# Performance work log

Measured on AMD Instinct MI355X. Metric: run time of the kernel, lower is better.

The kernel has to match this reference:

```python
import jax, jax.numpy as jnp
import numpy as np

B, P, D, K, OUT = 16, 2048, 64, 16, 128


def setup_inputs() -> dict:
    key = jax.random.key(0)
    k1, k2, k3 = jax.random.split(key, 3)
    x = jax.random.normal(k1, (B * P, D), dtype=jnp.float32)
    pos = jax.random.normal(k2, (B * P, 3), dtype=jnp.float32)
    batch = jnp.repeat(jnp.arange(B, dtype=jnp.int64), P)  # sorted segment ids
    # Linear(2*D -> OUT), torch convention W: [out, in]
    W = jax.random.normal(k3, (OUT, 2 * D), dtype=jnp.float32) / np.sqrt(2 * D)
    b = jnp.zeros((OUT,), dtype=jnp.float32)
    return {"x": x, "pos": pos, "batch": batch, "W": W, "b": b}


def _knn_idx(xb):
    # xb: [P, D] one cloud; returns [P, K] indices of K nearest neighbors (self excluded)
    sq = jnp.sum(xb * xb, axis=-1)  # [P]
    d2 = sq[:, None] + sq[None, :] - 2.0 * (xb @ xb.T)  # [P, P]
    d2 = d2 + jnp.eye(P, dtype=xb.dtype) * jnp.asarray(1e10, xb.dtype)  # loop=False
    _, idx = jax.lax.top_k(-d2, K)  # smallest distances
    return idx


def reference(x, pos, batch, W, b):
    # batch is uniform segments of size P (sorted), so reshape is equivalent
    xb = x.reshape(B, P, D)
    idx = jax.vmap(_knn_idx)(xb)  # [B, P, K]
    # gather neighbor features per cloud
    xj = jax.vmap(lambda f, i: f[i])(xb, idx)  # [B, P, K, D]
    xi = jnp.broadcast_to(xb[:, :, None, :], (B, P, K, D))
    e = jnp.concatenate([xi, xj - xi], axis=-1)  # [B, P, K, 2D]
    h = jnp.einsum('bpkd,od->bpko', e, W) + b  # edge MLP
    out = jnp.max(h, axis=2)  # max aggregation over neighbors -> [B, P, OUT]
    out = jax.nn.relu(out)
    return out.reshape(B * P, OUT)
```

## Files before the change

kernel.cpp:

```cpp
#include <hip/hip_runtime.h>

typedef __bf16 bf16x8 __attribute__((ext_vector_type(8)));
typedef float  f32x4  __attribute__((ext_vector_type(4)));

#define NBAT 16
#define NP   2048
#define ND   64
#define NOUT 128
#define NK   16
#define RT   16
#define HSTR 2052

static __device__ __forceinline__ unsigned short f2bf(float f) {
    unsigned u = __float_as_uint(f);
    u += 0x7FFF + ((u >> 16) & 1);
    return (unsigned short)(u >> 16);
}
static __device__ __forceinline__ int lanes_below(unsigned long long m) {
    return (int)__builtin_amdgcn_mbcnt_hi((unsigned)(m >> 32),
             __builtin_amdgcn_mbcnt_lo((unsigned)m, 0u));
}
static __device__ __forceinline__ unsigned long long umin64(unsigned long long a, unsigned long long b){ return a < b ? a : b; }
static __device__ __forceinline__ unsigned long long umax64(unsigned long long a, unsigned long long b){ return a < b ? b : a; }

static __device__ __forceinline__ void bitonic_sort128_u64(unsigned long long &k0,
                                                           unsigned long long &k1, int lane) {
#pragma unroll
    for (int k = 2; k <= 64; k <<= 1) {
#pragma unroll
        for (int j = k >> 1; j >= 1; j >>= 1) {
            bool lower = ((lane & j) == 0);
            bool up0 = (k == 64) ? true  : ((lane & k) == 0);
            bool up1 = (k == 64) ? false : ((lane & k) == 0);
            unsigned long long o0 = __shfl_xor(k0, j, 64);
            k0 = (up0 == lower) ? umin64(k0, o0) : umax64(k0, o0);
            unsigned long long o1 = __shfl_xor(k1, j, 64);
            k1 = (up1 == lower) ? umin64(k1, o1) : umax64(k1, o1);
        }
    }
    { unsigned long long mn = umin64(k0, k1), mx = umax64(k0, k1); k0 = mn; k1 = mx; }
#pragma unroll
    for (int j = 32; j >= 1; j >>= 1) {
        bool lower = ((lane & j) == 0);
        unsigned long long o0 = __shfl_xor(k0, j, 64);
        k0 = lower ? umin64(k0, o0) : umax64(k0, o0);
        unsigned long long o1 = __shfl_xor(k1, j, 64);
        k1 = lower ? umin64(k1, o1) : umax64(k1, o1);
    }
}

static __device__ __forceinline__ float
refine_d(const float* __restrict__ x, int gr, int gcbase, int jc) {
    const float* xr = x + (size_t)gr * ND;
    const float* xc = x + (size_t)(gcbase + jc) * ND;
    double s0 = 0.0, s1 = 0.0;
#pragma unroll
    for (int k8 = 0; k8 < 8; ++k8) {
        float4 a = *(const float4*)(xr + k8 * 8);
        float4 b = *(const float4*)(xc + k8 * 8);
        float4 a2 = *(const float4*)(xr + k8 * 8 + 4);
        float4 b2 = *(const float4*)(xc + k8 * 8 + 4);
        double e0 = (double)a.x - (double)b.x;
        double e1 = (double)a.y - (double)b.y;
        double e2 = (double)a.z - (double)b.z;
        double e3 = (double)a.w - (double)b.w;
        s0 = fma(e0, e0, s0); s0 = fma(e1, e1, s0);
        s0 = fma(e2, e2, s0); s0 = fma(e3, e3, s0);
        double f0 = (double)a2.x - (double)b2.x;
        double f1 = (double)a2.y - (double)b2.y;
        double f2 = (double)a2.z - (double)b2.z;
        double f3 = (double)a2.w - (double)b2.w;
        s1 = fma(f0, f0, s1); s1 = fma(f1, f1, s1);
        s1 = fma(f2, f2, s1); s1 = fma(f3, f3, s1);
    }
    return (float)(s0 + s1);
}

static __device__ __forceinline__ void cvt_hilo(const float* __restrict__ p,
                                                bf16x8 &hi, bf16x8 &lo) {
    float4 a = *(const float4*)p, b = *(const float4*)(p + 4);
    float f[8] = {a.x, a.y, a.z, a.w, b.x, b.y, b.z, b.w};
#pragma unroll
    for (int i = 0; i < 8; ++i) {
        __bf16 h = (__bf16)f[i];
        hi[i] = h;
        lo[i] = (__bf16)(f[i] - (float)h);
    }
}

__global__ void __launch_bounds__(256)
prep_k(const float* __restrict__ x,
       const float* __restrict__ W,
       const float* __restrict__ bias,
       float* __restrict__ sq, float* __restrict__ U,
       float* __restrict__ V,  unsigned short* __restrict__ xb16)
{
    const int blk = blockIdx.x, tid = threadIdx.x;
    const int R0b = blk * 64;
    const int w  = tid >> 6, l = tid & 63;
    const int l15 = l & 15, lg = l >> 4, kc = lg * 8;

    bf16x8 wh[2][4], wl[2][4];
#pragma unroll
    for (int tt = 0; tt < 2; ++tt) {
        const float* wb = W + (size_t)((w + tt * 4) * 16 + l15) * (2 * ND) + kc;
#pragma unroll
        for (int p = 0; p < 4; ++p)
            cvt_hilo(wb + p * 32, wh[tt][p], wl[tt][p]);
    }
    const int o0a = w * 16 + lg * 4;
    const int o0b = (w + 4) * 16 + lg * 4;
    float4 boa = *(const float4*)(bias + o0a);
    float4 bob = *(const float4*)(bias + o0b);

#pragma unroll 1
    for (int s4 = 0; s4 < 4; ++s4) {
        const int R0 = R0b + s4 * 16;

        {
            int r = tid >> 4, c = (tid & 15) * 4;
            float4 v = *(const float4*)(x + (size_t)(R0 + r) * ND + c);
            ushort4 hb;
            hb.x = f2bf(v.x); hb.y = f2bf(v.y); hb.z = f2bf(v.z); hb.w = f2bf(v.w);
            *(ushort4*)(xb16 + (size_t)(R0 + r) * ND + c) = hb;
        }
        if (tid < 128) {
            int r = tid >> 3, seg = tid & 7;
            const float* p = x + (size_t)(R0 + r) * ND + seg * 8;
            float4 a = *(const float4*)(p);
            float4 b = *(const float4*)(p + 4);
            double s = (double)a.x * a.x + (double)a.y * a.y +
                       (double)a.z * a.z + (double)a.w * a.w +
                       (double)b.x * b.x + (double)b.y * b.y +
                       (double)b.z * b.z + (double)b.w * b.w;
            s += __shfl_xor(s, 1, 64);
            s += __shfl_xor(s, 2, 64);
            s += __shfl_xor(s, 4, 64);
            if (seg == 0) sq[R0 + r] = (float)s;
        }

        const float* xr = x + (size_t)(R0 + l15) * ND + kc;
        bf16x8 bh0, bl0, bh1, bl1;
        cvt_hilo(xr,      bh0, bl0);
        cvt_hilo(xr + 32, bh1, bl1);

#pragma unroll
        for (int tt = 0; tt < 2; ++tt) {
            f32x4 accP = {0.f, 0.f, 0.f, 0.f};
            f32x4 accV = {0.f, 0.f, 0.f, 0.f};
            accP = __builtin_amdgcn_mfma_f32_16x16x32_bf16(wh[tt][0], bh0, accP, 0, 0, 0);
            accP = __builtin_amdgcn_mfma_f32_16x16x32_bf16(wh[tt][0], bl0, accP, 0, 0, 0);
            accP = __builtin_amdgcn_mfma_f32_16x16x32_bf16(wl[tt][0], bh0, accP, 0, 0, 0);
            accP = __builtin_amdgcn_mfma_f32_16x16x32_bf16(wh[tt][1], bh1, accP, 0, 0, 0);
            accP = __builtin_amdgcn_mfma_f32_16x16x32_bf16(wh[tt][1], bl1, accP, 0, 0, 0);
            accP = __builtin_amdgcn_mfma_f32_16x16x32_bf16(wl[tt][1], bh1, accP, 0, 0, 0);
            accV = __builtin_amdgcn_mfma_f32_16x16x32_bf16(wh[tt][2], bh0, accV, 0, 0, 0);
            accV = __builtin_amdgcn_mfma_f32_16x16x32_bf16(wh[tt][2], bl0, accV, 0, 0, 0);
            accV = __builtin_amdgcn_mfma_f32_16x16x32_bf16(wl[tt][2], bh0, accV, 0, 0, 0);
            accV = __builtin_amdgcn_mfma_f32_16x16x32_bf16(wh[tt][3], bh1, accV, 0, 0, 0);
            accV = __builtin_amdgcn_mfma_f32_16x16x32_bf16(wh[tt][3], bl1, accV, 0, 0, 0);
            accV = __builtin_amdgcn_mfma_f32_16x16x32_bf16(wl[tt][3], bh1, accV, 0, 0, 0);

            const int o0 = tt ? o0b : o0a;
            float4 bo = tt ? bob : boa;
            float4 uu, vv;
            uu.x = accP[0] - accV[0] + bo.x;  vv.x = accV[0];
            uu.y = accP[1] - accV[1] + bo.y;  vv.y = accV[1];
            uu.z = accP[2] - accV[2] + bo.z;  vv.z = accV[2];
            uu.w = accP[3] - accV[3] + bo.w;  vv.w = accV[3];
            *(float4*)(U + (size_t)(R0 + l15) * NOUT + o0) = uu;
            *(float4*)(V + (size_t)(R0 + l15) * NOUT + o0) = vv;
        }
    }
}

__global__ void __launch_bounds__(1024, 2)
knn_k(const float* __restrict__ x,
      const unsigned short* __restrict__ xb16,
      const float* __restrict__ sq,
      const float* __restrict__ U,
      const float* __restrict__ V,
      float* __restrict__ out)
{
    extern __shared__ __align__(16) unsigned char smem[];
    unsigned short* d2h = (unsigned short*)smem;
    __shared__ unsigned short cbuf[16][128];

    const int q   = blockIdx.x;
    const int xcd = q & 7;
    const int k_  = q >> 3;
    const int bb  = xcd * 2 + (k_ >> 7);
    const int rt  = k_ & 127;
    const int R0l = rt * RT;
    const int R0g = bb * NP + R0l;
    const int tid = threadIdx.x;
    const int w   = tid >> 6;
    const int l   = tid & 63;
    const int l15 = l & 15, lg = l >> 4, kc = lg * 8;

    const unsigned short* nr = xb16 + (size_t)(R0g + l15) * ND + kc;
    bf16x8 n0 = *(const bf16x8*)(nr);
    bf16x8 n1 = *(const bf16x8*)(nr + 32);
    const float sqrow = sq[R0g + l15];

    const unsigned short* xbb = xb16 + (size_t)bb * NP * ND;
    const float* sqb = sq + bb * NP;

#pragma unroll 4
    for (int t = 0; t < 8; ++t) {
        const int cb = (w * 8 + t) * 16;
        const unsigned short* ar = xbb + (size_t)(cb + l15) * ND + kc;
        bf16x8 a0 = *(const bf16x8*)(ar);
        bf16x8 a1 = *(const bf16x8*)(ar + 32);
        f32x4 acc = {0.f, 0.f, 0.f, 0.f};
        acc = __builtin_amdgcn_mfma_f32_16x16x32_bf16(a0, n0, acc, 0, 0, 0);
        acc = __builtin_amdgcn_mfma_f32_16x16x32_bf16(a1, n1, acc, 0, 0, 0);
        const int jb4 = cb + lg * 4;
        float4 sq4 = *(const float4*)(sqb + jb4);
        unsigned short hh[4];
#pragma unroll
        for (int i = 0; i < 4; ++i) {
            float sqc = (i == 0) ? sq4.x : (i == 1) ? sq4.y : (i == 2) ? sq4.z : sq4.w;
            float d2 = fmaxf(fmaf(-2.f, acc[i], sqrow + sqc), 0.f);
            unsigned short h = __builtin_bit_cast(unsigned short, (_Float16)d2);
            if (R0l + l15 == jb4 + i) h = 0x7C00;
            hh[i] = h;
        }
        ushort4 hv; hv.x = hh[0]; hv.y = hh[1]; hv.z = hh[2]; hv.w = hh[3];
        *(ushort4*)(d2h + (size_t)l15 * HSTR + jb4) = hv;
    }
    __syncthreads();

    const int gcbase = bb * NP;
    {
        const int r  = w;
        const int gr = R0g + r;
        const unsigned short* rowp = d2h + (size_t)r * HSTR;

        unsigned int h[32];
#pragma unroll
        for (int s = 0; s < 8; ++s) {
            ushort4 hv = *(const ushort4*)(rowp + (s * 64 + l) * 4);
            h[s*4+0] = hv.x; h[s*4+1] = hv.y; h[s*4+2] = hv.z; h[s*4+3] = hv.w;
        }
        unsigned int mnh = h[0];
#pragma unroll
        for (int i = 1; i < 32; ++i) mnh = (h[i] < mnh) ? h[i] : mnh;

        unsigned int t16 = 0;
#pragma unroll
        for (int b = 15; b >= 0; --b) {
            unsigned int cand = t16 | (1u << b);
            int c = __popcll(__ballot(mnh < cand));
            if (c < 16) t16 = cand;
        }
        float tf = (float)__builtin_bit_cast(_Float16, (unsigned short)t16) + 1.0f;
        unsigned int tauh =
            (unsigned int)__builtin_bit_cast(unsigned short, (_Float16)tf) + 1u;

        unsigned int packed = 0; int cnt = 0;
#pragma unroll
        for (int i = 0; i < 32; ++i) {
            if (h[i] <= tauh) {
                if (cnt < 4) packed |= (unsigned)i << (5 * cnt);
                ++cnt;
            }
        }
        bool ovf = (__ballot(cnt > 4) != 0ull);

        cbuf[w][l]      = 0xFFFF;
        cbuf[w][64 + l] = 0xFFFF;
        int total;
        if (!ovf) {
            int inc = cnt;
#pragma unroll
            for (int off = 1; off < 64; off <<= 1) {
                int nv = __shfl_up(inc, off, 64);
                if (l >= off) inc += nv;
            }
            int excl = inc - cnt;
            total = __shfl(inc, 63, 64);
#pragma unroll
            for (int kk = 0; kk < 4; ++kk) {
                if (kk < cnt && excl + kk < 128) {
                    int slot = (packed >> (5 * kk)) & 31;
                    cbuf[w][excl + kk] =
                        (unsigned short)(256 * (slot >> 2) + 4 * l + (slot & 3));
                }
            }
        } else {
            int base = 0;
#pragma unroll 1
            for (int i = 0; i < 32; ++i) {
                bool pred = (h[i] <= tauh);
                unsigned long long m = __ballot(pred);
                int pos = base + lanes_below(m);
                if (pred && pos < 128)
                    cbuf[w][pos] = (unsigned short)(256 * (i >> 2) + 4 * l + (i & 3));
                base += __popcll(m);
            }
            total = base;
        }
        asm volatile("s_waitcnt lgkmcnt(0)" ::: "memory");
        __builtin_amdgcn_sched_barrier(0);

        const float* Vb = V + (size_t)bb * NP * NOUT;
        float mv0 = -1e30f, mv1 = -1e30f;
        int jc = cbuf[w][l];

        bool fast = (total <= 64);
        unsigned long long win_m = 0ull;
        if (fast) {
            unsigned int dbits = 0xFFFFFFFFu;
            if (jc != 0xFFFF)
                dbits = __float_as_uint(refine_d(x, gr, gcbase, jc));

            unsigned int T = 0;
#pragma unroll
            for (int b = 30; b >= 0; --b) {
                unsigned int cand = T | (1u << b);
                int c = __popcll(__ballot(dbits < cand));
                if (c < 16) T = cand;
            }
            unsigned long long less_m = __ballot(dbits < T);
            int c_less = __popcll(less_m);
            int need = 16 - c_less;
            unsigned long long tie_m = __ballot(dbits == T);
            if (__popcll(tie_m) == need) {
                win_m = less_m | tie_m;
            } else {
                fast = false;
            }
        }

        if (fast) {
            int jns[NK];
            unsigned long long mm = win_m;
#pragma unroll
            for (int n = 0; n < NK; ++n) {
                int ln = __ffsll((long long)mm) - 1;
                jns[n] = __builtin_amdgcn_readlane(jc, ln);
                mm &= mm - 1;
            }
            float2 vv[NK];
#pragma unroll
            for (int n = 0; n < NK; ++n)
                vv[n] = *(const float2*)(Vb + (size_t)jns[n] * NOUT + (l << 1));
#pragma unroll
            for (int n = 0; n < NK; ++n) {
                mv0 = fmaxf(mv0, vv[n].x);
                mv1 = fmaxf(mv1, vv[n].y);
            }
        } else {
            int jc1 = cbuf[w][64 + l];
            unsigned long long rk0 = (jc != 0xFFFF)
                ? ((((unsigned long long)__float_as_uint(refine_d(x, gr, gcbase, jc))) << 11) | (unsigned)jc)
                : ~0ull;
            unsigned long long rk1 = (jc1 != 0xFFFF)
                ? ((((unsigned long long)__float_as_uint(refine_d(x, gr, gcbase, jc1))) << 11) | (unsigned)jc1)
                : ~0ull;
            bitonic_sort128_u64(rk0, rk1, l);
            int nbr = (int)(rk0 & 2047u);
            int jns[NK];
#pragma unroll
            for (int n = 0; n < NK; ++n)
                jns[n] = __builtin_amdgcn_readlane(nbr, n);
            float2 vv[NK];
#pragma unroll
            for (int n = 0; n < NK; ++n)
                vv[n] = *(const float2*)(Vb + (size_t)jns[n] * NOUT + (l << 1));
#pragma unroll
            for (int n = 0; n < NK; ++n) {
                mv0 = fmaxf(mv0, vv[n].x);
                mv1 = fmaxf(mv1, vv[n].y);
            }
        }

        float2 uu = *(const float2*)(U + (size_t)gr * NOUT + (l << 1));
        float2 ov;
        ov.x = fmaxf(uu.x + mv0, 0.f);
        ov.y = fmaxf(uu.y + mv1, 0.f);
        *(float2*)(out + (size_t)gr * NOUT + (l << 1)) = ov;
    }
}

extern "C" void kernel_launch(void* const* d_in, const int* in_sizes, int n_in,
                              void* d_out, int out_size, void* d_ws, size_t ws_size,
                              hipStream_t stream) {
    const float* x    = (const float*)d_in[0];
    const float* W    = (const float*)d_in[3];
    const float* bias = (const float*)d_in[4];
    float* out = (float*)d_out;

    float* sq = (float*)d_ws;
    float* U  = sq + NBAT * NP;
    float* V  = U  + (size_t)NBAT * NP * NOUT;
    unsigned short* xb16 = (unsigned short*)(V + (size_t)NBAT * NP * NOUT);

    prep_k<<<512, 256, 0, stream>>>(x, W, bias, sq, U, V, xb16);

    const int lds_bytes = RT * HSTR * 2;
    (void)hipFuncSetAttribute((const void*)knn_k,
                        hipFuncAttributeMaxDynamicSharedMemorySize, lds_bytes);
    knn_k<<<2048, 1024, lds_bytes, stream>>>(x, xb16, sq, U, V, out);
}
```

Before: 159.5 us.

## Halve knn block to 8 waves, each handling two rows with interleaved selection

The knn kernel now launches 512 threads per block instead of 1024. Each wave computes 16 column tiles of the distance matrix instead of 8, and later selects neighbours for two query rows at once, interleaving the ballot searches, the fp64 refinement and the V gathers for both rows to expose more ILP. The coarse threshold search now runs over 10 bits of the fp16 key instead of 16. This cuts per-row serial ballot latency and fits more blocks per CU, but raises register pressure, and the fallback path now runs serially over both rows whenever either row misses the fast path.

```diff
diff --git a/kernel.cpp b/kernel.cpp
--- a/kernel.cpp
+++ b/kernel.cpp
@@ -56,8 +56,8 @@
     double s0 = 0.0, s1 = 0.0;
 #pragma unroll
     for (int k8 = 0; k8 < 8; ++k8) {
-        float4 a = *(const float4*)(xr + k8 * 8);
-        float4 b = *(const float4*)(xc + k8 * 8);
+        float4 a  = *(const float4*)(xr + k8 * 8);
+        float4 b  = *(const float4*)(xc + k8 * 8);
         float4 a2 = *(const float4*)(xr + k8 * 8 + 4);
         float4 b2 = *(const float4*)(xc + k8 * 8 + 4);
         double e0 = (double)a.x - (double)b.x;
@@ -116,7 +116,6 @@
 #pragma unroll 1
     for (int s4 = 0; s4 < 4; ++s4) {
         const int R0 = R0b + s4 * 16;
-
         {
             int r = tid >> 4, c = (tid & 15) * 4;
             float4 v = *(const float4*)(x + (size_t)(R0 + r) * ND + c);
@@ -138,12 +137,10 @@
             s += __shfl_xor(s, 4, 64);
             if (seg == 0) sq[R0 + r] = (float)s;
         }
-
         const float* xr = x + (size_t)(R0 + l15) * ND + kc;
         bf16x8 bh0, bl0, bh1, bl1;
         cvt_hilo(xr,      bh0, bl0);
         cvt_hilo(xr + 32, bh1, bl1);
-
 #pragma unroll
         for (int tt = 0; tt < 2; ++tt) {
             f32x4 accP = {0.f, 0.f, 0.f, 0.f};
@@ -160,7 +157,6 @@
             accV = __builtin_amdgcn_mfma_f32_16x16x32_bf16(wh[tt][3], bh1, accV, 0, 0, 0);
             accV = __builtin_amdgcn_mfma_f32_16x16x32_bf16(wh[tt][3], bl1, accV, 0, 0, 0);
             accV = __builtin_amdgcn_mfma_f32_16x16x32_bf16(wl[tt][3], bh1, accV, 0, 0, 0);
-
             const int o0 = tt ? o0b : o0a;
             float4 bo = tt ? bob : boa;
             float4 uu, vv;
@@ -174,7 +170,7 @@
     }
 }
 
-__global__ void __launch_bounds__(1024, 2)
+__global__ void __launch_bounds__(512, 2)
 knn_k(const float* __restrict__ x,
       const unsigned short* __restrict__ xb16,
       const float* __restrict__ sq,
@@ -184,7 +180,7 @@
 {
     extern __shared__ __align__(16) unsigned char smem[];
     unsigned short* d2h = (unsigned short*)smem;
-    __shared__ unsigned short cbuf[16][128];
+    __shared__ unsigned short cbuf[8][2][128];
 
     const int q   = blockIdx.x;
     const int xcd = q & 7;
@@ -207,8 +203,8 @@
     const float* sqb = sq + bb * NP;
 
 #pragma unroll 4
-    for (int t = 0; t < 8; ++t) {
-        const int cb = (w * 8 + t) * 16;
+    for (int t = 0; t < 16; ++t) {
+        const int cb = (w * 16 + t) * 16;
         const unsigned short* ar = xbb + (size_t)(cb + l15) * ND + kc;
         bf16x8 a0 = *(const bf16x8*)(ar);
         bf16x8 a1 = *(const bf16x8*)(ar + 32);
@@ -232,156 +228,265 @@
     __syncthreads();
 
     const int gcbase = bb * NP;
+    const int rA = w, rB = w + 8;
+    const int grA = R0g + rA, grB = R0g + rB;
+    const unsigned short* rpA = d2h + (size_t)rA * HSTR;
+    const unsigned short* rpB = d2h + (size_t)rB * HSTR;
+
+    unsigned int hA[32], hB[32];
+#pragma unroll
+    for (int s = 0; s < 8; ++s) {
+        ushort4 a = *(const ushort4*)(rpA + (s * 64 + l) * 4);
+        ushort4 b = *(const ushort4*)(rpB + (s * 64 + l) * 4);
+        hA[s*4+0] = a.x; hA[s*4+1] = a.y; hA[s*4+2] = a.z; hA[s*4+3] = a.w;
+        hB[s*4+0] = b.x; hB[s*4+1] = b.y; hB[s*4+2] = b.z; hB[s*4+3] = b.w;
+    }
+    unsigned int mnA = hA[0], mnB = hB[0];
+#pragma unroll
+    for (int i = 1; i < 32; ++i) {
+        mnA = (hA[i] < mnA) ? hA[i] : mnA;
+        mnB = (hB[i] < mnB) ? hB[i] : mnB;
+    }
+
+    unsigned int m6A = mnA >> 6, m6B = mnB >> 6;
+    unsigned int tA = 0, tB = 0;
+#pragma unroll
+    for (int b = 9; b >= 0; --b) {
+        unsigned int cA = tA | (1u << b);
+        unsigned int cB = tB | (1u << b);
+        int nA = __popcll(__ballot(m6A < cA));
+        int nB = __popcll(__ballot(m6B < cB));
+        if (nA < 16) tA = cA;
+        if (nB < 16) tB = cB;
+    }
+    float tfA = (float)__builtin_bit_cast(_Float16, (unsigned short)((tA << 6) | 0x3F)) + 1.0f;
+    float tfB = (float)__builtin_bit_cast(_Float16, (unsigned short)((tB << 6) | 0x3F)) + 1.0f;
+    unsigned int tauA = (unsigned int)__builtin_bit_cast(unsigned short, (_Float16)tfA) + 1u;
+    unsigned int tauB = (unsigned int)__builtin_bit_cast(unsigned short, (_Float16)tfB) + 1u;
+
+    unsigned int pkA = 0, pkB = 0; int cntA = 0, cntB = 0;
+#pragma unroll
+    for (int i = 0; i < 32; ++i) {
+        if (hA[i] <= tauA) { if (cntA < 4) pkA |= (unsigned)i << (5 * cntA); ++cntA; }
+        if (hB[i] <= tauB) { if (cntB < 4) pkB |= (unsigned)i << (5 * cntB); ++cntB; }
+    }
+    bool ovfA = (__ballot(cntA > 4) != 0ull);
+    bool ovfB = (__ballot(cntB > 4) != 0ull);
+
+    cbuf[w][0][l] = 0xFFFF; cbuf[w][0][64 + l] = 0xFFFF;
+    cbuf[w][1][l] = 0xFFFF; cbuf[w][1][64 + l] = 0xFFFF;
+    int totA, totB;
     {
-        const int r  = w;
-        const int gr = R0g + r;
-        const unsigned short* rowp = d2h + (size_t)r * HSTR;
-
-        unsigned int h[32];
-#pragma unroll
-        for (int s = 0; s < 8; ++s) {
-            ushort4 hv = *(const ushort4*)(rowp + (s * 64 + l) * 4);
-            h[s*4+0] = hv.x; h[s*4+1] = hv.y; h[s*4+2] = hv.z; h[s*4+3] = hv.w;
-        }
-        unsigned int mnh = h[0];
-#pragma unroll
-        for (int i = 1; i < 32; ++i) mnh = (h[i] < mnh) ? h[i] : mnh;
-
-        unsigned int t16 = 0;
-#pragma unroll
-        for (int b = 15; b >= 0; --b) {
-            unsigned int cand = t16 | (1u << b);
-            int c = __popcll(__ballot(mnh < cand));
-            if (c < 16) t16 = cand;
-        }
-        float tf = (float)__builtin_bit_cast(_Float16, (unsigned short)t16) + 1.0f;
-        unsigned int tauh =
-            (unsigned int)__builtin_bit_cast(unsigned short, (_Float16)tf) + 1u;
-
-        unsigned int packed = 0; int cnt = 0;
-#pragma unroll
-        for (int i = 0; i < 32; ++i) {
-            if (h[i] <= tauh) {
-                if (cnt < 4) packed |= (unsigned)i << (5 * cnt);
-                ++cnt;
-            }
-        }
-        bool ovf = (__ballot(cnt > 4) != 0ull);
-
-        cbuf[w][l]      = 0xFFFF;
-        cbuf[w][64 + l] = 0xFFFF;
-        int total;
-        if (!ovf) {
-            int inc = cnt;
-#pragma unroll
-            for (int off = 1; off < 64; off <<= 1) {
-                int nv = __shfl_up(inc, off, 64);
-                if (l >= off) inc += nv;
-            }
-            int excl = inc - cnt;
-            total = __shfl(inc, 63, 64);
-#pragma unroll
-            for (int kk = 0; kk < 4; ++kk) {
-                if (kk < cnt && excl + kk < 128) {
-                    int slot = (packed >> (5 * kk)) & 31;
-                    cbuf[w][excl + kk] =
-                        (unsigned short)(256 * (slot >> 2) + 4 * l + (slot & 3));
+        int iA = cntA, iB = cntB;
+#pragma unroll
+        for (int off = 1; off < 64; off <<= 1) {
+            int uA = __shfl_up(iA, off, 64);
+            int uB = __shfl_up(iB, off, 64);
+            if (l >= off) { iA += uA; iB += uB; }
+        }
+        int exA = iA - cntA, exB = iB - cntB;
+        totA = __shfl(iA, 63, 64);
+        totB = __shfl(iB, 63, 64);
+        if (!ovfA) {
+#pragma unroll
+            for (int kk = 0; kk < 4; ++kk)
+                if (kk < cntA && exA + kk < 128) {
+                    int s = (pkA >> (5 * kk)) & 31;
+                    cbuf[w][0][exA + kk] = (unsigned short)(256 * (s >> 2) + 4 * l + (s & 3));
                 }
-            }
         } else {
             int base = 0;
 #pragma unroll 1
             for (int i = 0; i < 32; ++i) {
-                bool pred = (h[i] <= tauh);
-                unsigned long long m = __ballot(pred);
+                bool p = (hA[i] <= tauA);
+                unsigned long long m = __ballot(p);
                 int pos = base + lanes_below(m);
-                if (pred && pos < 128)
-                    cbuf[w][pos] = (unsigned short)(256 * (i >> 2) + 4 * l + (i & 3));
+                if (p && pos < 128)
+                    cbuf[w][0][pos] = (unsigned short)(256 * (i >> 2) + 4 * l + (i & 3));
                 base += __popcll(m);
             }
-            total = base;
-        }
-        asm volatile("s_waitcnt lgkmcnt(0)" ::: "memory");
-        __builtin_amdgcn_sched_barrier(0);
-
-        const float* Vb = V + (size_t)bb * NP * NOUT;
-        float mv0 = -1e30f, mv1 = -1e30f;
-        int jc = cbuf[w][l];
-
-        bool fast = (total <= 64);
-        unsigned long long win_m = 0ull;
-        if (fast) {
-            unsigned int dbits = 0xFFFFFFFFu;
-            if (jc != 0xFFFF)
-                dbits = __float_as_uint(refine_d(x, gr, gcbase, jc));
-
-            unsigned int T = 0;
-#pragma unroll
-            for (int b = 30; b >= 0; --b) {
-                unsigned int cand = T | (1u << b);
-                int c = __popcll(__ballot(dbits < cand));
-                if (c < 16) T = cand;
+            totA = base;
+        }
+        if (!ovfB) {
+#pragma unroll
+            for (int kk = 0; kk < 4; ++kk)
+                if (kk < cntB && exB + kk < 128) {
+                    int s = (pkB >> (5 * kk)) & 31;
+                    cbuf[w][1][exB + kk] = (unsigned short)(256 * (s >> 2) + 4 * l + (s & 3));
+                }
+        } else {
+            int base = 0;
+#pragma unroll 1
+            for (int i = 0; i < 32; ++i) {
+                bool p = (hB[i] <= tauB);
+                unsigned long long m = __ballot(p);
+                int pos = base + lanes_below(m);
+                if (p && pos < 128)
+                    cbuf[w][1][pos] = (unsigned short)(256 * (i >> 2) + 4 * l + (i & 3));
+                base += __popcll(m);
             }
-            unsigned long long less_m = __ballot(dbits < T);
-            int c_less = __popcll(less_m);
-            int need = 16 - c_less;
-            unsigned long long tie_m = __ballot(dbits == T);
-            if (__popcll(tie_m) == need) {
-                win_m = less_m | tie_m;
+            totB = base;
+        }
+    }
+    asm volatile("s_waitcnt lgkmcnt(0)" ::: "memory");
+    __builtin_amdgcn_sched_barrier(0);
+
+    const float* Vb = V + (size_t)bb * NP * NOUT;
+    int jcA = cbuf[w][0][l];
+    int jcB = cbuf[w][1][l];
+
+    int jsA = (jcA == 0xFFFF) ? 0 : jcA;
+    int jsB = (jcB == 0xFFFF) ? 0 : jcB;
+    unsigned int dbA, dbB;
+    {
+        const float* xrA = x + (size_t)grA * ND;
+        const float* xcA = x + (size_t)(gcbase + jsA) * ND;
+        const float* xrB = x + (size_t)grB * ND;
+        const float* xcB = x + (size_t)(gcbase + jsB) * ND;
+        double a0 = 0.0, a1 = 0.0, b0 = 0.0, b1 = 0.0;
+#pragma unroll
+        for (int k8 = 0; k8 < 8; ++k8) {
+            float4 ra  = *(const float4*)(xrA + k8 * 8);
+            float4 ca  = *(const float4*)(xcA + k8 * 8);
+            float4 ra2 = *(const float4*)(xrA + k8 * 8 + 4);
+            float4 ca2 = *(const float4*)(xcA + k8 * 8 + 4);
+            float4 rb  = *(const float4*)(xrB + k8 * 8);
+            float4 cb2 = *(const float4*)(xcB + k8 * 8);
+            float4 rb2 = *(const float4*)(xrB + k8 * 8 + 4);
+            float4 cb3 = *(const float4*)(xcB + k8 * 8 + 4);
+            double e0 = (double)ra.x - (double)ca.x;
+            double e1 = (double)ra.y - (double)ca.y;
+            double e2 = (double)ra.z - (double)ca.z;
+            double e3 = (double)ra.w - (double)ca.w;
+            a0 = fma(e0, e0, a0); a0 = fma(e1, e1, a0);
+            a0 = fma(e2, e2, a0); a0 = fma(e3, e3, a0);
+            double f0 = (double)ra2.x - (double)ca2.x;
+            double f1 = (double)ra2.y - (double)ca2.y;
+            double f2 = (double)ra2.z - (double)ca2.z;
+            double f3 = (double)ra2.w - (double)ca2.w;
+            a1 = fma(f0, f0, a1); a1 = fma(f1, f1, a1);
+            a1 = fma(f2, f2, a1); a1 = fma(f3, f3, a1);
+            double g0 = (double)rb.x - (double)cb2.x;
+            double g1 = (double)rb.y - (double)cb2.y;
+            double g2 = (double)rb.z - (double)cb2.z;
+            double g3 = (double)rb.w - (double)cb2.w;
+            b0 = fma(g0, g0, b0); b0 = fma(g1, g1, b0);
+            b0 = fma(g2, g2, b0); b0 = fma(g3, g3, b0);
+            double h0 = (double)rb2.x - (double)cb3.x;
+            double h1 = (double)rb2.y - (double)cb3.y;
+            double h2 = (double)rb2.z - (double)cb3.z;
+            double h3 = (double)rb2.w - (double)cb3.w;
+            b1 = fma(h0, h0, b1); b1 = fma(h1, h1, b1);
+            b1 = fma(h2, h2, b1); b1 = fma(h3, h3, b1);
+        }
+        dbA = (jcA == 0xFFFF) ? 0xFFFFFFFFu : __float_as_uint((float)(a0 + a1));
+        dbB = (jcB == 0xFFFF) ? 0xFFFFFFFFu : __float_as_uint((float)(b0 + b1));
+    }
+
+    unsigned int TA = 0, TB = 0;
+#pragma unroll
+    for (int b = 30; b >= 0; --b) {
+        unsigned int cA = TA | (1u << b);
+        unsigned int cB = TB | (1u << b);
+        int nA = __popcll(__ballot(dbA < cA));
+        int nB = __popcll(__ballot(dbB < cB));
+        if (nA < 16) TA = cA;
+        if (nB < 16) TB = cB;
+    }
+    unsigned long long lessA = __ballot(dbA < TA);
+    unsigned long long lessB = __ballot(dbB < TB);
+    int needA = 16 - __popcll(lessA);
+    int needB = 16 - __popcll(lessB);
+    unsigned long long tieA = __ballot(dbA == TA);
+    unsigned long long tieB = __ballot(dbB == TB);
+    bool fastA = (totA <= 64) && (__popcll(tieA) == needA);
+    bool fastB = (totB <= 64) && (__popcll(tieB) == needB);
+
+    float mvA0 = -1e30f, mvA1 = -1e30f, mvB0 = -1e30f, mvB1 = -1e30f;
+
+    if (fastA && fastB) {
+        unsigned long long wmA = lessA | tieA;
+        unsigned long long wmB = lessB | tieB;
+        int jnA[NK], jnB[NK];
+#pragma unroll
+        for (int n = 0; n < NK; ++n) {
+            int lnA = __ffsll((long long)wmA) - 1; wmA &= wmA - 1;
+            int lnB = __ffsll((long long)wmB) - 1; wmB &= wmB - 1;
+            jnA[n] = __builtin_amdgcn_readlane(jcA, lnA);
+            jnB[n] = __builtin_amdgcn_readlane(jcB, lnB);
+        }
+        float2 vA[NK], vB[NK];
+#pragma unroll
+        for (int n = 0; n < NK; ++n) {
+            vA[n] = *(const float2*)(Vb + (size_t)jnA[n] * NOUT + (l << 1));
+            vB[n] = *(const float2*)(Vb + (size_t)jnB[n] * NOUT + (l << 1));
+        }
+#pragma unroll
+        for (int n = 0; n < NK; ++n) {
+            mvA0 = fmaxf(mvA0, vA[n].x); mvA1 = fmaxf(mvA1, vA[n].y);
+            mvB0 = fmaxf(mvB0, vB[n].x); mvB1 = fmaxf(mvB1, vB[n].y);
+        }
+    } else {
+#pragma unroll 1
+        for (int half = 0; half < 2; ++half) {
+            bool fa  = half ? fastB : fastA;
+            int  jc  = half ? jcB : jcA;
+            int  gr  = half ? grB : grA;
+            int  tot = half ? totB : totA;
+            unsigned long long wm = half ? (lessB | tieB) : (lessA | tieA);
+            float m0 = -1e30f, m1 = -1e30f;
+            if (fa) {
+                int jns[NK];
+                unsigned long long mm = wm;
+#pragma unroll
+                for (int n = 0; n < NK; ++n) {
+                    int ln = __ffsll((long long)mm) - 1; mm &= mm - 1;
+                    jns[n] = __builtin_amdgcn_readlane(jc, ln);
+                }
+                float2 vv[NK];
+#pragma unroll
+                for (int n = 0; n < NK; ++n)
+                    vv[n] = *(const float2*)(Vb + (size_t)jns[n] * NOUT + (l << 1));
+#pragma unroll
+                for (int n = 0; n < NK; ++n) {
+                    m0 = fmaxf(m0, vv[n].x); m1 = fmaxf(m1, vv[n].y);
+                }
             } else {
-                fast = false;
+                int jc1 = cbuf[w][half][64 + l];
+                unsigned long long rk0 = (jc != 0xFFFF)
+                    ? ((((unsigned long long)__float_as_uint(refine_d(x, gr, gcbase, jc))) << 11) | (unsigned)jc)
+                    : ~0ull;
+                unsigned long long rk1 = (jc1 != 0xFFFF)
+                    ? ((((unsigned long long)__float_as_uint(refine_d(x, gr, gcbase, jc1))) << 11) | (unsigned)jc1)
+                    : ~0ull;
+                bitonic_sort128_u64(rk0, rk1, l);
+                int nbr = (int)(rk0 & 2047u);
+                int jns[NK];
+#pragma unroll
+                for (int n = 0; n < NK; ++n)
+                    jns[n] = __builtin_amdgcn_readlane(nbr, n);
+                float2 vv[NK];
+#pragma unroll
+                for (int n = 0; n < NK; ++n)
+                    vv[n] = *(const float2*)(Vb + (size_t)jns[n] * NOUT + (l << 1));
+#pragma unroll
+                for (int n = 0; n < NK; ++n) {
+                    m0 = fmaxf(m0, vv[n].x); m1 = fmaxf(m1, vv[n].y);
+                }
             }
-        }
-
-        if (fast) {
-            int jns[NK];
-            unsigned long long mm = win_m;
-#pragma unroll
-            for (int n = 0; n < NK; ++n) {
-                int ln = __ffsll((long long)mm) - 1;
-                jns[n] = __builtin_amdgcn_readlane(jc, ln);
-                mm &= mm - 1;
-            }
-            float2 vv[NK];
-#pragma unroll
-            for (int n = 0; n < NK; ++n)
-                vv[n] = *(const float2*)(Vb + (size_t)jns[n] * NOUT + (l << 1));
-#pragma unroll
-            for (int n = 0; n < NK; ++n) {
-                mv0 = fmaxf(mv0, vv[n].x);
-                mv1 = fmaxf(mv1, vv[n].y);
-            }
-        } else {
-            int jc1 = cbuf[w][64 + l];
-            unsigned long long rk0 = (jc != 0xFFFF)
-                ? ((((unsigned long long)__float_as_uint(refine_d(x, gr, gcbase, jc))) << 11) | (unsigned)jc)
-                : ~0ull;
-            unsigned long long rk1 = (jc1 != 0xFFFF)
-                ? ((((unsigned long long)__float_as_uint(refine_d(x, gr, gcbase, jc1))) << 11) | (unsigned)jc1)
-                : ~0ull;
-            bitonic_sort128_u64(rk0, rk1, l);
-            int nbr = (int)(rk0 & 2047u);
-            int jns[NK];
-#pragma unroll
-            for (int n = 0; n < NK; ++n)
-                jns[n] = __builtin_amdgcn_readlane(nbr, n);
-            float2 vv[NK];
-#pragma unroll
-            for (int n = 0; n < NK; ++n)
-                vv[n] = *(const float2*)(Vb + (size_t)jns[n] * NOUT + (l << 1));
-#pragma unroll
-            for (int n = 0; n < NK; ++n) {
-                mv0 = fmaxf(mv0, vv[n].x);
-                mv1 = fmaxf(mv1, vv[n].y);
-            }
-        }
-
-        float2 uu = *(const float2*)(U + (size_t)gr * NOUT + (l << 1));
-        float2 ov;
-        ov.x = fmaxf(uu.x + mv0, 0.f);
-        ov.y = fmaxf(uu.y + mv1, 0.f);
-        *(float2*)(out + (size_t)gr * NOUT + (l << 1)) = ov;
-    }
+            if (half) { mvB0 = m0; mvB1 = m1; } else { mvA0 = m0; mvA1 = m1; }
+        }
+    }
+
+    float2 uA = *(const float2*)(U + (size_t)grA * NOUT + (l << 1));
+    float2 uB = *(const float2*)(U + (size_t)grB * NOUT + (l << 1));
+    float2 oA, oB;
+    oA.x = fmaxf(uA.x + mvA0, 0.f);
+    oA.y = fmaxf(uA.y + mvA1, 0.f);
+    oB.x = fmaxf(uB.x + mvB0, 0.f);
+    oB.y = fmaxf(uB.y + mvB1, 0.f);
+    *(float2*)(out + (size_t)grA * NOUT + (l << 1)) = oA;
+    *(float2*)(out + (size_t)grB * NOUT + (l << 1)) = oB;
 }
 
 extern "C" void kernel_launch(void* const* d_in, const int* in_sizes, int n_in,
@@ -402,5 +507,5 @@
     const int lds_bytes = RT * HSTR * 2;
     (void)hipFuncSetAttribute((const void*)knn_k,
                         hipFuncAttributeMaxDynamicSharedMemorySize, lds_bytes);
-    knn_k<<<2048, 1024, lds_bytes, stream>>>(x, xb16, sq, U, V, out);
-}
+    knn_k<<<2048, 512, lds_bytes, stream>>>(x, xb16, sq, U, V, out);
+}
```

Measured after the change: 220.1 us. 38.0% more time.
